# Kernel optimization log

Measured on AMD Instinct MI355X. Metric: run time of the kernel, lower is better.

## Reference

```python
import jax, jax.numpy as jnp
import numpy as np

ORDER = 24
N_POINTS = 524288


def setup_inputs() -> dict:
    key = jax.random.key(0)
    k1, k2 = jax.random.split(key)
    xyz = jax.random.uniform(k1, (N_POINTS, 3), dtype=jnp.float32)
    coeffs = jax.random.normal(k2, (ORDER ** 3,), dtype=jnp.float32) * 0.1
    return {"xyz": xyz, "coeffs": coeffs}


def reference(xyz, coeffs):
    # Faithful to: sum_{i,j,k} c[i,j,k] * sin(2pi i x) * sin(2pi j y) * sin(2pi k z)
    # but with per-axis sin tables computed once (O(order) transcendentals per point)
    # and the triple sum expressed as chained contractions (GEMM-like).
    order = ORDER
    C = coeffs.reshape(order, order, order)  # c[i,j,k]
    n = jnp.arange(order, dtype=xyz.dtype)   # frequencies 0..order-1 (i=0 row is all zeros)
    two_pi = jnp.asarray(2.0 * np.pi, dtype=xyz.dtype)
    S = jnp.sin(two_pi * xyz[:, :, None] * n)  # [N, 3, order]
    Sx, Sy, Sz = S[:, 0, :], S[:, 1, :], S[:, 2, :]  # each [N, order]
    A = jnp.einsum('nk,ijk->nij', Sz, C)   # [N, order, order]
    B = jnp.einsum('nj,nij->ni', Sy, A)    # [N, order]
    return jnp.einsum('ni,ni->n', Sx, B)   # [N]
```

## Files before the change

kernel.cpp:

```cpp
#include <hip/hip_runtime.h>

typedef _Float16 f16x2 __attribute__((ext_vector_type(2)));
typedef _Float16 f16x8 __attribute__((ext_vector_type(8)));
typedef __fp16   fp16v2 __attribute__((ext_vector_type(2)));
typedef float    f32x4  __attribute__((ext_vector_type(4)));
typedef float    f32x16 __attribute__((ext_vector_type(16)));
typedef unsigned int u32x4 __attribute__((ext_vector_type(4)));

#define TROWSTR 28

__device__ __forceinline__ f16x2 pk2(float lo, float hi) {
    fp16v2 p = __builtin_amdgcn_cvt_pkrtz(lo, hi);
    return __builtin_bit_cast(f16x2, p);
}
__device__ __forceinline__ unsigned int pkbits(f16x2 a, f16x2 b) {
    f16x2 r = a * b;
    return __builtin_bit_cast(unsigned int, r);
}

__global__ __launch_bounds__(256) void prep_B(const float* __restrict__ coeffs,
                                              f16x8* __restrict__ wsB)
{
    int chunk = blockIdx.x * 256 + threadIdx.x;
    int s = chunk >> 6, l = chunk & 63;
    int i = l & 31, h = l >> 5;
    f16x8 v;
    if (i < 24) {
        const float* src = coeffs + i * 576 + 16 * s + 8 * h;
#pragma unroll
        for (int e = 0; e < 8; ++e) v[e] = (_Float16)src[e];
    } else {
#pragma unroll
        for (int e = 0; e < 8; ++e) v[e] = (_Float16)0.f;
    }
    wsB[chunk] = v;
}

__global__ __launch_bounds__(256, 2) void fourier_main(
    const float* __restrict__ xyz,
    const f16x8* __restrict__ wsB,
    float* __restrict__ out)
{
    __shared__ __align__(16) float Tl[4 * 64 * TROWSTR];

    const int tid  = threadIdx.x;
    const int wave = tid >> 6;
    const int lane = tid & 63;
    const int h    = lane >> 5;
    const int mr   = lane & 31;
    const bool hb  = (h != 0);

    const int p0 = (blockIdx.x * 4 + wave) * 64;

    const float xv = xyz[3 * (p0 + lane)];

    f16x8 bt[36];
#pragma unroll
    for (int s = 1; s < 36; ++s) bt[s] = wsB[s * 64 + lane];

    float syp[2], syc[2], c2y[2];
    f16x2 szR[2][3][4];

#pragma unroll
    for (int mt = 0; mt < 2; ++mt) {
        int p = p0 + mt * 32 + mr;
        float y = xyz[3 * p + 1];
        float z = xyz[3 * p + 2];

        float s1y = __builtin_amdgcn_sinf(y);
        float c1y = __builtin_amdgcn_cosf(y);
        c2y[mt] = 2.f * c1y;
        syc[mt] = hb ? s1y : 0.f;
        syp[mt] = hb ? 0.f : -s1y;

        float s1 = __builtin_amdgcn_sinf(z);
        float c1 = __builtin_amdgcn_cosf(z);
        float w8 = __builtin_amdgcn_fractf(8.f * z);
        float s8 = __builtin_amdgcn_sinf(w8);
        float c8 = __builtin_amdgcn_cosf(w8);
        float s16 = 2.f * s8 * c8;
        float c16 = fmaf(2.f * c8, c8, -1.f);
        float c2z = 2.f * c1;

#pragma unroll
        for (int t = 0; t < 3; ++t) {
            float sk, ck;
            if (t == 0) { sk = hb ? s8  : 0.f;  ck = hb ? c8  : 1.f;  }
            if (t == 1) { sk = hb ? s16 : s8;   ck = hb ? c16 : c8;   }
            if (t == 2) { sk = hb ? 0.f : s16;  ck = hb ? 1.f : c16;  }
            float v[8];
            v[0] = sk;
            v[1] = fmaf(sk, c1, ck * s1);
#pragma unroll
            for (int e = 2; e < 8; ++e) v[e] = fmaf(c2z, v[e - 1], -v[e - 2]);
#pragma unroll
            for (int q = 0; q < 4; ++q) szR[mt][t][q] = pk2(v[2 * q], v[2 * q + 1]);
        }
    }

    f32x16 acc0 = {};
    f32x16 acc1 = {};

#pragma unroll
    for (int s = 1; s < 36; ++s) {
        const int t = (2 * s) % 3;
        {
            f16x2 hy2 = pk2(syc[0], syc[0]);
            u32x4 aw;
            aw[0] = pkbits(hy2, szR[0][t][0]);
            aw[1] = pkbits(hy2, szR[0][t][1]);
            aw[2] = pkbits(hy2, szR[0][t][2]);
            aw[3] = pkbits(hy2, szR[0][t][3]);
            f16x8 a = __builtin_bit_cast(f16x8, aw);
            acc0 = __builtin_amdgcn_mfma_f32_32x32x16_f16(a, bt[s], acc0, 0, 0, 0);
        }
        {
            f16x2 hy2 = pk2(syc[1], syc[1]);
            u32x4 aw;
            aw[0] = pkbits(hy2, szR[1][t][0]);
            aw[1] = pkbits(hy2, szR[1][t][1]);
            aw[2] = pkbits(hy2, szR[1][t][2]);
            aw[3] = pkbits(hy2, szR[1][t][3]);
            f16x8 a = __builtin_bit_cast(f16x8, aw);
            acc1 = __builtin_amdgcn_mfma_f32_32x32x16_f16(a, bt[s], acc1, 0, 0, 0);
        }
        if (s < 35) {
#pragma unroll
            for (int mt = 0; mt < 2; ++mt) {
                float t1 = fmaf(c2y[mt], syc[mt], -syp[mt]);
                if ((s % 3) == 2) {
                    syp[mt] = syc[mt]; syc[mt] = t1;
                } else {
                    bool stay = ((s % 3) == 0) ? !hb : hb;
                    float np = stay ? syp[mt] : syc[mt];
                    float nc = stay ? syc[mt] : t1;
                    syp[mt] = np; syc[mt] = nc;
                }
            }
        }
    }

    float* Tw = Tl + wave * (64 * TROWSTR);
    if (mr < 24) {
#pragma unroll
        for (int r = 0; r < 16; ++r) {
            int row = (r & 3) + 8 * (r >> 2) + 4 * h;
            Tw[row * TROWSTR + mr]        = acc0[r];
            Tw[(32 + row) * TROWSTR + mr] = acc1[r];
        }
    }
    asm volatile("s_waitcnt lgkmcnt(0)" ::: "memory");

    {
        int p = p0 + lane;
        float s1  = __builtin_amdgcn_sinf(xv);
        float c1  = __builtin_amdgcn_cosf(xv);
        const float c2x = 2.f * c1;
        const f32x4* T4 = (const f32x4*)(Tw + lane * TROWSTR);
        f32x4 tv0 = T4[0], tv1 = T4[1], tv2 = T4[2];
        f32x4 tv3 = T4[3], tv4 = T4[4], tv5 = T4[5];
        float tv[24];
#pragma unroll
        for (int q = 0; q < 4; ++q) {
            tv[q]      = tv0[q]; tv[4 + q]  = tv1[q]; tv[8 + q]  = tv2[q];
            tv[12 + q] = tv3[q]; tv[16 + q] = tv4[q]; tv[20 + q] = tv5[q];
        }
        float sp = 0.f, sc = s1, res = 0.f;
#pragma unroll
        for (int i = 1; i < 24; ++i) {
            res = fmaf(sc, tv[i], res);
            float nx = fmaf(c2x, sc, -sp);
            sp = sc; sc = nx;
        }
        out[p] = res;
    }
}

extern "C" void kernel_launch(void* const* d_in, const int* in_sizes, int n_in,
                              void* d_out, int out_size, void* d_ws, size_t ws_size,
                              hipStream_t stream) {
    const float* xyz    = (const float*)d_in[0];
    const float* coeffs = (const float*)d_in[1];
    float* out = (float*)d_out;
    f16x8* wsB = (f16x8*)d_ws;

    prep_B<<<9, 256, 0, stream>>>(coeffs, wsB);

    const int n = in_sizes[0] / 3;
    const int grid = n / 256;
    fourier_main<<<grid, 256, 0, stream>>>(xyz, wsB, out);
}
```

Baseline: 31.00 us.

## Fuse coefficient prep into main kernel, stage B tiles in shared memory

```diff
diff --git a/kernel.cpp b/kernel.cpp
--- a/kernel.cpp
+++ b/kernel.cpp
@@ -3,11 +3,10 @@
 typedef _Float16 f16x2 __attribute__((ext_vector_type(2)));
 typedef _Float16 f16x8 __attribute__((ext_vector_type(8)));
 typedef __fp16   fp16v2 __attribute__((ext_vector_type(2)));
-typedef float    f32x4  __attribute__((ext_vector_type(4)));
 typedef float    f32x16 __attribute__((ext_vector_type(16)));
 typedef unsigned int u32x4 __attribute__((ext_vector_type(4)));
 
-#define TROWSTR 28
+#define TROWSTR 25
 
 __device__ __forceinline__ f16x2 pk2(float lo, float hi) {
     fp16v2 p = __builtin_amdgcn_cvt_pkrtz(lo, hi);
@@ -18,30 +17,12 @@
     return __builtin_bit_cast(unsigned int, r);
 }
 
-__global__ __launch_bounds__(256) void prep_B(const float* __restrict__ coeffs,
-                                              f16x8* __restrict__ wsB)
-{
-    int chunk = blockIdx.x * 256 + threadIdx.x;
-    int s = chunk >> 6, l = chunk & 63;
-    int i = l & 31, h = l >> 5;
-    f16x8 v;
-    if (i < 24) {
-        const float* src = coeffs + i * 576 + 16 * s + 8 * h;
-#pragma unroll
-        for (int e = 0; e < 8; ++e) v[e] = (_Float16)src[e];
-    } else {
-#pragma unroll
-        for (int e = 0; e < 8; ++e) v[e] = (_Float16)0.f;
-    }
-    wsB[chunk] = v;
-}
-
-__global__ __launch_bounds__(256, 2) void fourier_main(
+__global__ __launch_bounds__(256, 4) void fourier_fused(
     const float* __restrict__ xyz,
-    const f16x8* __restrict__ wsB,
+    const float* __restrict__ coeffs,
     float* __restrict__ out)
 {
-    __shared__ __align__(16) float Tl[4 * 64 * TROWSTR];
+    __shared__ __align__(16) f16x8 Bl[2240];
 
     const int tid  = threadIdx.x;
     const int wave = tid >> 6;
@@ -54,9 +35,25 @@
 
     const float xv = xyz[3 * (p0 + lane)];
 
-    f16x8 bt[36];
 #pragma unroll
-    for (int s = 1; s < 36; ++s) bt[s] = wsB[s * 64 + lane];
+    for (int pass = 0; pass < 9; ++pass) {
+        int chunk = pass * 256 + tid;
+        if (chunk < 2240) {
+            int s = 1 + (chunk >> 6);
+            int l = chunk & 63;
+            int i = l & 31, hh = l >> 5;
+            f16x8 v;
+            if (i < 24) {
+                const float* src = coeffs + i * 576 + 16 * s + 8 * hh;
+#pragma unroll
+                for (int e = 0; e < 8; ++e) v[e] = (_Float16)src[e];
+            } else {
+#pragma unroll
+                for (int e = 0; e < 8; ++e) v[e] = (_Float16)0.f;
+            }
+            Bl[chunk] = v;
+        }
+    }
 
     float syp[2], syc[2], c2y[2];
     f16x2 szR[2][3][4];
@@ -101,8 +98,11 @@
     f32x16 acc0 = {};
     f32x16 acc1 = {};
 
+    __syncthreads();
+
 #pragma unroll
     for (int s = 1; s < 36; ++s) {
+        f16x8 bs = Bl[(s - 1) * 64 + lane];
         const int t = (2 * s) % 3;
         {
             f16x2 hy2 = pk2(syc[0], syc[0]);
@@ -112,7 +112,7 @@
             aw[2] = pkbits(hy2, szR[0][t][2]);
             aw[3] = pkbits(hy2, szR[0][t][3]);
             f16x8 a = __builtin_bit_cast(f16x8, aw);
-            acc0 = __builtin_amdgcn_mfma_f32_32x32x16_f16(a, bt[s], acc0, 0, 0, 0);
+            acc0 = __builtin_amdgcn_mfma_f32_32x32x16_f16(a, bs, acc0, 0, 0, 0);
         }
         {
             f16x2 hy2 = pk2(syc[1], syc[1]);
@@ -122,7 +122,7 @@
             aw[2] = pkbits(hy2, szR[1][t][2]);
             aw[3] = pkbits(hy2, szR[1][t][3]);
             f16x8 a = __builtin_bit_cast(f16x8, aw);
-            acc1 = __builtin_amdgcn_mfma_f32_32x32x16_f16(a, bt[s], acc1, 0, 0, 0);
+            acc1 = __builtin_amdgcn_mfma_f32_32x32x16_f16(a, bs, acc1, 0, 0, 0);
         }
         if (s < 35) {
 #pragma unroll
@@ -140,7 +140,9 @@
         }
     }
 
-    float* Tw = Tl + wave * (64 * TROWSTR);
+    __syncthreads();
+
+    float* Tw = (float*)Bl + wave * (64 * TROWSTR);
     if (mr < 24) {
 #pragma unroll
         for (int r = 0; r < 16; ++r) {
@@ -153,22 +155,14 @@
 
     {
         int p = p0 + lane;
-        float s1  = __builtin_amdgcn_sinf(xv);
-        float c1  = __builtin_amdgcn_cosf(xv);
+        float s1 = __builtin_amdgcn_sinf(xv);
+        float c1 = __builtin_amdgcn_cosf(xv);
         const float c2x = 2.f * c1;
-        const f32x4* T4 = (const f32x4*)(Tw + lane * TROWSTR);
-        f32x4 tv0 = T4[0], tv1 = T4[1], tv2 = T4[2];
-        f32x4 tv3 = T4[3], tv4 = T4[4], tv5 = T4[5];
-        float tv[24];
-#pragma unroll
-        for (int q = 0; q < 4; ++q) {
-            tv[q]      = tv0[q]; tv[4 + q]  = tv1[q]; tv[8 + q]  = tv2[q];
-            tv[12 + q] = tv3[q]; tv[16 + q] = tv4[q]; tv[20 + q] = tv5[q];
-        }
+        const float* Tr = Tw + lane * TROWSTR;
         float sp = 0.f, sc = s1, res = 0.f;
 #pragma unroll
         for (int i = 1; i < 24; ++i) {
-            res = fmaf(sc, tv[i], res);
+            res = fmaf(sc, Tr[i], res);
             float nx = fmaf(c2x, sc, -sp);
             sp = sc; sc = nx;
         }
@@ -182,11 +176,8 @@
     const float* xyz    = (const float*)d_in[0];
     const float* coeffs = (const float*)d_in[1];
     float* out = (float*)d_out;
-    f16x8* wsB = (f16x8*)d_ws;
-
-    prep_B<<<9, 256, 0, stream>>>(coeffs, wsB);
 
     const int n = in_sizes[0] / 3;
     const int grid = n / 256;
-    fourier_main<<<grid, 256, 0, stream>>>(xyz, wsB, out);
+    fourier_fused<<<grid, 256, 0, stream>>>(xyz, coeffs, out);
 }
```

After: 34.30 us. 1.11x slower.

## Loop each wave over eight 32-point tiles to amortize coefficient register loads

Applied to the files above, without the earlier changes.

```diff
diff --git a/kernel.cpp b/kernel.cpp
--- a/kernel.cpp
+++ b/kernel.cpp
@@ -3,11 +3,10 @@
 typedef _Float16 f16x2 __attribute__((ext_vector_type(2)));
 typedef _Float16 f16x8 __attribute__((ext_vector_type(8)));
 typedef __fp16   fp16v2 __attribute__((ext_vector_type(2)));
-typedef float    f32x4  __attribute__((ext_vector_type(4)));
 typedef float    f32x16 __attribute__((ext_vector_type(16)));
 typedef unsigned int u32x4 __attribute__((ext_vector_type(4)));
 
-#define TROWSTR 28
+#define TROWSTR 25
 
 __device__ __forceinline__ f16x2 pk2(float lo, float hi) {
     fp16v2 p = __builtin_amdgcn_cvt_pkrtz(lo, hi);
@@ -41,7 +40,7 @@
     const f16x8* __restrict__ wsB,
     float* __restrict__ out)
 {
-    __shared__ __align__(16) float Tl[4 * 64 * TROWSTR];
+    __shared__ __align__(16) float Tl[4 * 32 * TROWSTR];
 
     const int tid  = threadIdx.x;
     const int wave = tid >> 6;
@@ -50,38 +49,43 @@
     const int mr   = lane & 31;
     const bool hb  = (h != 0);
 
-    const int p0 = (blockIdx.x * 4 + wave) * 64;
-
-    const float xv = xyz[3 * (p0 + lane)];
+    const int pw = (blockIdx.x * 4 + wave) * 256;
 
     f16x8 bt[36];
 #pragma unroll
     for (int s = 1; s < 36; ++s) bt[s] = wsB[s * 64 + lane];
 
-    float syp[2], syc[2], c2y[2];
-    f16x2 szR[2][3][4];
+    float cx = xyz[3 * (pw + mr) + 0];
+    float cy = xyz[3 * (pw + mr) + 1];
+    float cz = xyz[3 * (pw + mr) + 2];
 
-#pragma unroll
-    for (int mt = 0; mt < 2; ++mt) {
-        int p = p0 + mt * 32 + mr;
-        float y = xyz[3 * p + 1];
-        float z = xyz[3 * p + 2];
+    float* Tw = Tl + wave * (32 * TROWSTR);
 
-        float s1y = __builtin_amdgcn_sinf(y);
-        float c1y = __builtin_amdgcn_cosf(y);
-        c2y[mt] = 2.f * c1y;
-        syc[mt] = hb ? s1y : 0.f;
-        syp[mt] = hb ? 0.f : -s1y;
+#pragma unroll 1
+    for (int it = 0; it < 8; ++it) {
+        const int pp0 = pw + it * 32;
 
-        float s1 = __builtin_amdgcn_sinf(z);
-        float c1 = __builtin_amdgcn_cosf(z);
-        float w8 = __builtin_amdgcn_fractf(8.f * z);
+        int pn = (it < 7) ? (pp0 + 32 + mr) : (pw + mr);
+        float nx = xyz[3 * pn + 0];
+        float ny = xyz[3 * pn + 1];
+        float nz = xyz[3 * pn + 2];
+
+        float s1y = __builtin_amdgcn_sinf(cy);
+        float c1y = __builtin_amdgcn_cosf(cy);
+        float c2y = 2.f * c1y;
+        float syc = hb ? s1y : 0.f;
+        float syp = hb ? 0.f : -s1y;
+
+        float s1 = __builtin_amdgcn_sinf(cz);
+        float c1 = __builtin_amdgcn_cosf(cz);
+        float w8 = __builtin_amdgcn_fractf(8.f * cz);
         float s8 = __builtin_amdgcn_sinf(w8);
         float c8 = __builtin_amdgcn_cosf(w8);
         float s16 = 2.f * s8 * c8;
         float c16 = fmaf(2.f * c8, c8, -1.f);
         float c2z = 2.f * c1;
 
+        f16x2 szR[3][4];
 #pragma unroll
         for (int t = 0; t < 3; ++t) {
             float sk, ck;
@@ -94,85 +98,60 @@
 #pragma unroll
             for (int e = 2; e < 8; ++e) v[e] = fmaf(c2z, v[e - 1], -v[e - 2]);
 #pragma unroll
-            for (int q = 0; q < 4; ++q) szR[mt][t][q] = pk2(v[2 * q], v[2 * q + 1]);
+            for (int q = 0; q < 4; ++q) szR[t][q] = pk2(v[2 * q], v[2 * q + 1]);
         }
-    }
 
-    f32x16 acc0 = {};
-    f32x16 acc1 = {};
+        f32x16 acc = {};
 
 #pragma unroll
-    for (int s = 1; s < 36; ++s) {
-        const int t = (2 * s) % 3;
-        {
-            f16x2 hy2 = pk2(syc[0], syc[0]);
+        for (int s = 1; s < 36; ++s) {
+            const int t = (2 * s) % 3;
+            f16x2 hy2 = pk2(syc, syc);
             u32x4 aw;
-            aw[0] = pkbits(hy2, szR[0][t][0]);
-            aw[1] = pkbits(hy2, szR[0][t][1]);
-            aw[2] = pkbits(hy2, szR[0][t][2]);
-            aw[3] = pkbits(hy2, szR[0][t][3]);
+            aw[0] = pkbits(hy2, szR[t][0]);
+            aw[1] = pkbits(hy2, szR[t][1]);
+            aw[2] = pkbits(hy2, szR[t][2]);
+            aw[3] = pkbits(hy2, szR[t][3]);
             f16x8 a = __builtin_bit_cast(f16x8, aw);
-            acc0 = __builtin_amdgcn_mfma_f32_32x32x16_f16(a, bt[s], acc0, 0, 0, 0);
-        }
-        {
-            f16x2 hy2 = pk2(syc[1], syc[1]);
-            u32x4 aw;
-            aw[0] = pkbits(hy2, szR[1][t][0]);
-            aw[1] = pkbits(hy2, szR[1][t][1]);
-            aw[2] = pkbits(hy2, szR[1][t][2]);
-            aw[3] = pkbits(hy2, szR[1][t][3]);
-            f16x8 a = __builtin_bit_cast(f16x8, aw);
-            acc1 = __builtin_amdgcn_mfma_f32_32x32x16_f16(a, bt[s], acc1, 0, 0, 0);
-        }
-        if (s < 35) {
-#pragma unroll
-            for (int mt = 0; mt < 2; ++mt) {
-                float t1 = fmaf(c2y[mt], syc[mt], -syp[mt]);
+            acc = __builtin_amdgcn_mfma_f32_32x32x16_f16(a, bt[s], acc, 0, 0, 0);
+            if (s < 35) {
+                float t1 = fmaf(c2y, syc, -syp);
                 if ((s % 3) == 2) {
-                    syp[mt] = syc[mt]; syc[mt] = t1;
+                    syp = syc; syc = t1;
                 } else {
                     bool stay = ((s % 3) == 0) ? !hb : hb;
-                    float np = stay ? syp[mt] : syc[mt];
-                    float nc = stay ? syc[mt] : t1;
-                    syp[mt] = np; syc[mt] = nc;
+                    float np = stay ? syp : syc;
+                    float nc = stay ? syc : t1;
+                    syp = np; syc = nc;
                 }
             }
         }
-    }
 
-    float* Tw = Tl + wave * (64 * TROWSTR);
-    if (mr < 24) {
+        if (mr < 24) {
 #pragma unroll
-        for (int r = 0; r < 16; ++r) {
-            int row = (r & 3) + 8 * (r >> 2) + 4 * h;
-            Tw[row * TROWSTR + mr]        = acc0[r];
-            Tw[(32 + row) * TROWSTR + mr] = acc1[r];
+            for (int r = 0; r < 16; ++r) {
+                int row = (r & 3) + 8 * (r >> 2) + 4 * h;
+                Tw[row * TROWSTR + mr] = acc[r];
+            }
         }
-    }
-    asm volatile("s_waitcnt lgkmcnt(0)" ::: "memory");
+        asm volatile("s_waitcnt lgkmcnt(0)" ::: "memory");
 
-    {
-        int p = p0 + lane;
-        float s1  = __builtin_amdgcn_sinf(xv);
-        float c1  = __builtin_amdgcn_cosf(xv);
-        const float c2x = 2.f * c1;
-        const f32x4* T4 = (const f32x4*)(Tw + lane * TROWSTR);
-        f32x4 tv0 = T4[0], tv1 = T4[1], tv2 = T4[2];
-        f32x4 tv3 = T4[3], tv4 = T4[4], tv5 = T4[5];
-        float tv[24];
+        {
+            float sx1 = __builtin_amdgcn_sinf(cx);
+            float cx1 = __builtin_amdgcn_cosf(cx);
+            const float c2x = 2.f * cx1;
+            const float* Tr = Tw + mr * TROWSTR;
+            float sp = 0.f, sc = sx1, res = 0.f;
 #pragma unroll
-        for (int q = 0; q < 4; ++q) {
-            tv[q]      = tv0[q]; tv[4 + q]  = tv1[q]; tv[8 + q]  = tv2[q];
-            tv[12 + q] = tv3[q]; tv[16 + q] = tv4[q]; tv[20 + q] = tv5[q];
+            for (int i = 1; i < 24; ++i) {
+                res = fmaf(sc, Tr[i], res);
+                float nxr = fmaf(c2x, sc, -sp);
+                sp = sc; sc = nxr;
+            }
+            if (lane < 32) out[pp0 + mr] = res;
         }
-        float sp = 0.f, sc = s1, res = 0.f;
-#pragma unroll
-        for (int i = 1; i < 24; ++i) {
-            res = fmaf(sc, tv[i], res);
-            float nx = fmaf(c2x, sc, -sp);
-            sp = sc; sc = nx;
-        }
-        out[p] = res;
+
+        cx = nx; cy = ny; cz = nz;
     }
 }
 
@@ -187,6 +166,6 @@
     prep_B<<<9, 256, 0, stream>>>(coeffs, wsB);
 
     const int n = in_sizes[0] / 3;
-    const int grid = n / 256;
+    const int grid = n / 1024;
     fourier_main<<<grid, 256, 0, stream>>>(xyz, wsB, out);
 }
```

After: 32.08 us. 1.03x slower.
